# Performance work log

Hardware: AMD Instinct MI355X
Metric: run time of the kernel (lower is better)

The kernel has to match this reference:

```python
import jax, jax.numpy as jnp
import numpy as np

NUM_HEADS = 8

def setup_inputs() -> dict:
    key = jax.random.key(0)
    ks = jax.random.split(key, 7)
    B, H, W, C = 4, 56, 56, 256
    Nq = 1
    std = 0.02
    return {
        "x": jax.random.normal(ks[0], (B, H, W, C), jnp.float32),
        "cls_token": jax.random.normal(ks[1], (B, Nq, C), jnp.float32),
        "qkv_w": jax.random.normal(ks[2], (3 * C, C), jnp.float32) * std,
        "proj_w": jax.random.normal(ks[3], (C, C), jnp.float32) * std,
        "proj_b": jnp.zeros((C,), jnp.float32),
        "lepe_w": jax.random.normal(ks[4], (C, 1, 5, 5), jnp.float32) * std,
        "lepe_b": jnp.zeros((C,), jnp.float32),
    }

def reference(x, cls_token, qkv_w, proj_w, proj_b, lepe_w, lepe_b):
    B, H, W, C = x.shape
    N = H * W
    Nq = cls_token.shape[1]
    hd = C // NUM_HEADS
    scale = hd ** -0.5

    x_seq = x.reshape(B, N, C)
    x_cat = jnp.concatenate([cls_token, x_seq], axis=1)        # [B, Nq+N, C]

    qkv = x_cat @ qkv_w.T                                      # [B, Nq+N, 3C]
    qkv = qkv.reshape(B, Nq + N, 3, NUM_HEADS, hd)
    q, k, v = qkv[:, :, 0], qkv[:, :, 1], qkv[:, :, 2]         # [B, S, h, d]

    attn = jnp.einsum('bshd,bthd->bhst', q, k) * scale         # [B, h, S, S]
    attn = jax.nn.softmax(attn, axis=-1)
    out = jnp.einsum('bhst,bthd->bshd', attn, v).reshape(B, Nq + N, C)

    cls_out, x_out = out[:, :Nq], out[:, Nq:]

    # depthwise conv LePE on the raw spatial input
    x_nchw = jnp.transpose(x, (0, 3, 1, 2))                    # [B, C, H, W]
    lepe = jax.lax.conv_general_dilated(
        x_nchw, lepe_w, window_strides=(1, 1), padding='SAME',
        feature_group_count=C,
        dimension_numbers=('NCHW', 'OIHW', 'NCHW'))
    lepe = lepe + lepe_b[None, :, None, None]
    lepe = jnp.transpose(lepe, (0, 2, 3, 1)).reshape(B, N, C)

    x_out = (x_out + lepe) @ proj_w.T + proj_b
    cls_out = cls_out @ proj_w.T + proj_b
    return x_out.reshape(B, H, W, C), cls_out
```

## Files before the change

### kernel.cpp

```cpp
#include <hip/hip_runtime.h>
#include <math.h>

#define BB 4
#define HH 56
#define WW 56
#define CC 256
#define NN 3136
#define SS 3137
#define NH 8
#define HD 32
#define M_ROWS (BB * SS)
#define SPAD 3200
#define QSCALE (0.17677669529663687f * 1.4426950408889634f)
#define KT 128

typedef short short8 __attribute__((ext_vector_type(8)));
typedef short bf4    __attribute__((ext_vector_type(4)));
typedef float f32x4  __attribute__((ext_vector_type(4)));

static __device__ __forceinline__ unsigned short f2bf(float f) {
    union { float f; unsigned u; } a; a.f = f;
    unsigned r = a.u + 0x7FFF + ((a.u >> 16) & 1);
    return (unsigned short)(r >> 16);
}
static __device__ __forceinline__ float bf2f(unsigned short h) {
    union { unsigned u; float f; } a; a.u = ((unsigned)h) << 16; return a.f;
}

__global__ __launch_bounds__(256)
void pre(const float* __restrict__ cls, const float* __restrict__ qkv_w,
         const float* __restrict__ proj_w, const float* __restrict__ lepe_w,
         unsigned short* __restrict__ xb, unsigned short* __restrict__ wb,
         unsigned short* __restrict__ pwhi, unsigned short* __restrict__ pwlo,
         unsigned short* __restrict__ vt, float* __restrict__ wt,
         unsigned short* __restrict__ lepe)
{
    const int B0 = 192;
    const int B1 = B0 + 64;
    const int B2 = B1 + 64;
    const int B3 = B2 + 25;
    int blk = blockIdx.x, tid = threadIdx.x;
    if (blk < B0) {
        int row = blk * 4 + (tid >> 6);
        int c0 = (tid & 63) * 4;
        float4 v = *(const float4*)(qkv_w + (size_t)row * CC + c0);
        bf4 pk;
        pk[0] = (short)f2bf(v.x); pk[1] = (short)f2bf(v.y);
        pk[2] = (short)f2bf(v.z); pk[3] = (short)f2bf(v.w);
        *(bf4*)(wb + (size_t)row * CC + c0) = pk;
    } else if (blk < B1) {
        int row = (blk - B0) * 4 + (tid >> 6);
        int c0 = (tid & 63) * 4;
        float4 v = *(const float4*)(proj_w + (size_t)row * CC + c0);
        bf4 ph, pl;
        float vv[4] = {v.x, v.y, v.z, v.w};
        #pragma unroll
        for (int e = 0; e < 4; ++e) {
            unsigned short h = f2bf(vv[e]);
            ph[e] = (short)h;
            pl[e] = (short)f2bf(vv[e] - bf2f(h));
        }
        *(bf4*)(pwhi + (size_t)row * CC + c0) = ph;
        *(bf4*)(pwlo + (size_t)row * CC + c0) = pl;
    } else if (blk < B2) {
        int idx = blk - B1;
        int row = idx * 16 + (tid >> 4);
        int col = 3136 + (tid & 15) * 4;
        bf4 z = {};
        *(bf4*)(vt + (size_t)row * SPAD + col) = z;
    } else if (blk < B3) {
        int t = blk - B2;
        wt[(size_t)t * CC + tid] = lepe_w[(size_t)tid * 25 + t];
    } else {
        int b = blk - B3;
        xb[((size_t)b * SS) * CC + tid] = f2bf(cls[(size_t)b * CC + tid]);
        lepe[((size_t)b * SS) * CC + tid] = 0;
    }
}

__global__ __launch_bounds__(256)
void lepe_tiled(const float* __restrict__ x,
                const float* __restrict__ wt, const float* __restrict__ bias,
                unsigned short* __restrict__ lepe, unsigned short* __restrict__ xb)
{
    __shared__ unsigned short Xs[144][72];
    __shared__ float Wls[25][68];

    const int tid = threadIdx.x;
    const int bid = blockIdx.x;
    const int sp  = bid % 49;
    const int ct  = (bid / 49) & 3;
    const int b   = bid / 196;
    const int y0 = (sp / 7) * 8, x0 = (sp % 7) * 8;
    const int c0 = ct * 64;

    const int cq = tid & 15;
    const int pg = tid >> 4;

    #pragma unroll
    for (int r = 0; r < 9; ++r) {
        int seg = r * 16 + pg;
        int dy = seg / 12, dx = seg % 12;
        int yy = y0 + dy - 2, xc = x0 + dx - 2;
        bf4 v = {};
        if (yy >= 0 && yy < HH && xc >= 0 && xc < WW) {
            float4 f = *(const float4*)(x + (((size_t)b * HH + yy) * WW + xc) * CC
                                        + c0 + cq * 4);
            v[0] = (short)f2bf(f.x); v[1] = (short)f2bf(f.y);
            v[2] = (short)f2bf(f.z); v[3] = (short)f2bf(f.w);
        }
        *(bf4*)&Xs[seg][cq * 4] = v;
    }
    for (int idx = tid; idx < 1600; idx += 256) {
        int t = idx >> 6, c = idx & 63;
        Wls[t][c] = wt[(size_t)t * CC + c0 + c];
    }
    __syncthreads();

    float4 bq = *(const float4*)(bias + c0 + cq * 4);
    f32x4 acc[4];
    #pragma unroll
    for (int it = 0; it < 4; ++it) {
        acc[it][0] = bq.x; acc[it][1] = bq.y; acc[it][2] = bq.z; acc[it][3] = bq.w;
    }
    int hbase[4];
    #pragma unroll
    for (int it = 0; it < 4; ++it) {
        int pos = it * 16 + pg;
        hbase[it] = (pos >> 3) * 12 + (pos & 7);
    }

    #pragma unroll
    for (int it = 0; it < 4; ++it) {
        int pos = it * 16 + pg;
        int py = pos >> 3, px = pos & 7;
        uint2 dv = *(const uint2*)&Xs[(py + 2) * 12 + (px + 2)][cq * 4];
        *(uint2*)(xb + ((size_t)(b * SS + 1 + (y0 + py) * WW + (x0 + px))) * CC
                  + c0 + cq * 4) = dv;
    }

    #pragma unroll
    for (int t = 0; t < 25; ++t) {
        int dy = t / 5, dx = t % 5;
        float4 wq = *(const float4*)&Wls[t][cq * 4];
        #pragma unroll
        for (int it = 0; it < 4; ++it) {
            const unsigned short* xp = &Xs[hbase[it] + dy * 12 + dx][cq * 4];
            uint2 dv = *(const uint2*)xp;
            float e0 = __uint_as_float(dv.x << 16);
            float e1 = __uint_as_float(dv.x & 0xFFFF0000u);
            float e2 = __uint_as_float(dv.y << 16);
            float e3 = __uint_as_float(dv.y & 0xFFFF0000u);
            acc[it][0] += e0 * wq.x; acc[it][1] += e1 * wq.y;
            acc[it][2] += e2 * wq.z; acc[it][3] += e3 * wq.w;
        }
    }

    #pragma unroll
    for (int it = 0; it < 4; ++it) {
        int pos = it * 16 + pg;
        int py = pos >> 3, px = pos & 7;
        bf4 pk;
        pk[0] = (short)f2bf(acc[it][0]); pk[1] = (short)f2bf(acc[it][1]);
        pk[2] = (short)f2bf(acc[it][2]); pk[3] = (short)f2bf(acc[it][3]);
        *(bf4*)(lepe + ((size_t)(b * SS + 1 + (y0 + py) * WW + (x0 + px))) * CC
                + c0 + cq * 4) = pk;
    }
}

__global__ __launch_bounds__(256)
void qkv_mfma(const unsigned short* __restrict__ xb,
              const unsigned short* __restrict__ wb,
              unsigned short* __restrict__ qb, unsigned short* __restrict__ kb,
              unsigned short* __restrict__ vt)
{
    __shared__ unsigned short As[64][76];
    __shared__ unsigned short Bs[128][76];
    const int tid = threadIdx.x;
    const int w = tid >> 6, lane = tid & 63, lo = lane & 15, hi = lane >> 4;
    const int b0 = blockIdx.x / 50;
    const int s0blk = (blockIdx.x % 50) * 64;
    const int col0 = blockIdx.y * 128;
    const int wm = (w & 1) * 32, wn = (w >> 1) * 64;

    f32x4 acc[2][4] = {};

    const int arow = tid >> 3, ac8 = (tid & 7) * 8;
    const int brow = tid >> 3, bc8 = (tid & 7) * 8;

    short8 avr[2], bvr[4];
    #pragma unroll
    for (int i = 0; i < 2; ++i) {
        int row = arow + i * 32;
        short8 av = {};
        if (s0blk + row < SS)
            av = *(const short8*)(xb + (size_t)(b0 * SS + s0blk + row) * CC + ac8);
        avr[i] = av;
    }
    #pragma unroll
    for (int i = 0; i < 4; ++i)
        bvr[i] = *(const short8*)(wb + (size_t)(col0 + brow + i * 32) * CC + bc8);

    for (int k0 = 0; k0 < CC; k0 += 64) {
        __syncthreads();
        #pragma unroll
        for (int i = 0; i < 2; ++i)
            *(short8*)&As[arow + i * 32][ac8] = avr[i];
        #pragma unroll
        for (int i = 0; i < 4; ++i)
            *(short8*)&Bs[brow + i * 32][bc8] = bvr[i];
        __syncthreads();

        int kn = k0 + 64;
        if (kn < CC) {
            #pragma unroll
            for (int i = 0; i < 2; ++i) {
                int row = arow + i * 32;
                short8 av = {};
                if (s0blk + row < SS)
                    av = *(const short8*)(xb + (size_t)(b0 * SS + s0blk + row) * CC + kn + ac8);
                avr[i] = av;
            }
            #pragma unroll
            for (int i = 0; i < 4; ++i)
                bvr[i] = *(const short8*)(wb + (size_t)(col0 + brow + i * 32) * CC + kn + bc8);
        }

        #pragma unroll
        for (int kk = 0; kk < 64; kk += 32) {
            short8 af[2], bf_[4];
            #pragma unroll
            for (int m = 0; m < 2; ++m)
                af[m] = *(const short8*)&As[wm + m * 16 + lo][kk + hi * 8];
            #pragma unroll
            for (int n = 0; n < 4; ++n)
                bf_[n] = *(const short8*)&Bs[wn + n * 16 + lo][kk + hi * 8];
            #pragma unroll
            for (int m = 0; m < 2; ++m)
                #pragma unroll
                for (int n = 0; n < 4; ++n)
                    acc[m][n] = __builtin_amdgcn_mfma_f32_16x16x32_bf16(
                                    af[m], bf_[n], acc[m][n], 0, 0, 0);
        }
    }

    const int part = col0 >> 8;
    if (part < 2) {
        #pragma unroll
        for (int m = 0; m < 2; ++m) {
            #pragma unroll
            for (int rr = 0; rr < 4; ++rr) {
                int s = s0blk + wm + m * 16 + hi * 4 + rr;
                if (s >= SS) continue;
                size_t r = (size_t)(b0 * SS + s);
                #pragma unroll
                for (int n = 0; n < 4; ++n) {
                    int cc = (col0 + wn + n * 16 + lo) & 255;
                    float val = acc[m][n][rr];
                    if (part == 0) qb[r * CC + cc] = f2bf(val * QSCALE);
                    else           kb[r * CC + cc] = f2bf(val);
                }
            }
        }
    } else {
        #pragma unroll
        for (int m = 0; m < 2; ++m) {
            int s0 = s0blk + wm + m * 16 + hi * 4;
            if (s0 >= SS) continue;
            bool fast = (s0 + 3 < SS);
            #pragma unroll
            for (int n = 0; n < 4; ++n) {
                int cc = (col0 + wn + n * 16 + lo) & 255;
                int hh = cc >> 5, d = cc & 31;
                unsigned short* vrow = vt + (size_t)((b0 * NH + hh) * HD + d) * SPAD;
                if (fast) {
                    bf4 pk;
                    pk[0] = (short)f2bf(acc[m][n][0]);
                    pk[1] = (short)f2bf(acc[m][n][1]);
                    pk[2] = (short)f2bf(acc[m][n][2]);
                    pk[3] = (short)f2bf(acc[m][n][3]);
                    *(bf4*)(vrow + s0) = pk;
                } else {
                    for (int rr = 0; rr < 4 && s0 + rr < SS; ++rr)
                        vrow[s0 + rr] = f2bf(acc[m][n][rr]);
                }
            }
        }
    }
}

__global__ __launch_bounds__(256)
void attn_mfma(const unsigned short* __restrict__ qb,
               const unsigned short* __restrict__ kb,
               const unsigned short* __restrict__ vt,
               const unsigned short* __restrict__ lepe,
               unsigned short* __restrict__ ohi)
{
    __shared__ unsigned short Ks[KT][44];
    __shared__ unsigned short Vts[32][140];

    const int tid  = threadIdx.x;
    const int lane = tid & 63;
    const int w    = tid >> 6;
    const int lo   = lane & 15;
    const int hi   = lane >> 4;

    const int bid = blockIdx.x;
    const int h   = bid & 7;
    const int j   = bid >> 3;
    const int qc  = j % 25;
    const int b   = j / 25;
    const int q0w = qc * 128 + w * 32;

    short8 qa[2];
    #pragma unroll
    for (int qg = 0; qg < 2; ++qg) {
        int row = min(q0w + qg * 16 + lo, SS - 1);
        qa[qg] = *(const short8*)(qb + ((size_t)(b * SS + row)) * CC + h * HD + hi * 8);
    }

    f32x4 oacc[2][2] = {};
    f32x4 dacc[2] = {};
    bf4 ones;
    ones[0] = (short)0x3F80; ones[1] = (short)0x3F80;
    ones[2] = (short)0x3F80; ones[3] = (short)0x3F80;

    const int krow = tid >> 2, kd0 = (tid & 3) * 8;
    const int vrow = tid >> 4, vk0 = (tid & 15) * 8;
    const unsigned short* kp0 = kb + ((size_t)b * SS + krow) * CC + h * HD + kd0;
    const unsigned short* vp0 = vt + ((size_t)((b * NH + h) * HD + vrow)) * SPAD + vk0;

    short8 kv0 = *(const short8*)(kp0);
    short8 kv1 = *(const short8*)(kp0 + (size_t)64 * CC);
    short8 vv0 = *(const short8*)(vp0);
    short8 vv1 = *(const short8*)(vp0 + (size_t)16 * SPAD);

    for (int k0 = 0; k0 < SPAD; k0 += KT) {
        __syncthreads();
        *(short8*)&Ks[krow][kd0]       = kv0;
        *(short8*)&Ks[64 + krow][kd0]  = kv1;
        *(short8*)&Vts[vrow][vk0]      = vv0;
        *(short8*)&Vts[16 + vrow][vk0] = vv1;
        __syncthreads();

        int kn = k0 + KT;
        if (kn < SPAD) {
            short8 z = {};
            kv0 = (kn + krow < SS)      ? *(const short8*)(kp0 + (size_t)kn * CC)        : z;
            kv1 = (kn + 64 + krow < SS) ? *(const short8*)(kp0 + (size_t)(kn + 64) * CC) : z;
            vv0 = *(const short8*)(vp0 + kn);
            vv1 = *(const short8*)(vp0 + (size_t)16 * SPAD + kn);
        }

        #pragma unroll
        for (int g = 0; g < 8; ++g) {
            short8 kf = *(const short8*)&Ks[g * 16 + lo][hi * 8];
            bf4 vf0 = *(const bf4*)&Vts[lo][g * 16 + hi * 4];
            bf4 vf1 = *(const bf4*)&Vts[16 + lo][g * 16 + hi * 4];
            #pragma unroll
            for (int qg = 0; qg < 2; ++qg) {
                f32x4 st = __builtin_amdgcn_mfma_f32_16x16x32_bf16(
                               kf, qa[qg], (f32x4){0.f, 0.f, 0.f, 0.f}, 0, 0, 0);
                float p0 = __builtin_amdgcn_exp2f(st[0]);
                float p1 = __builtin_amdgcn_exp2f(st[1]);
                float p2 = __builtin_amdgcn_exp2f(st[2]);
                float p3 = __builtin_amdgcn_exp2f(st[3]);
                unsigned u01 = __builtin_amdgcn_perm(
                    __float_as_uint(p1), __float_as_uint(p0), 0x07060302u);
                unsigned u23 = __builtin_amdgcn_perm(
                    __float_as_uint(p3), __float_as_uint(p2), 0x07060302u);
                union { unsigned u[2]; bf4 s; } pf;
                pf.u[0] = u01; pf.u[1] = u23;
                oacc[qg][0] = __builtin_amdgcn_mfma_f32_16x16x16bf16_1k(
                                  vf0, pf.s, oacc[qg][0], 0, 0, 0);
                oacc[qg][1] = __builtin_amdgcn_mfma_f32_16x16x16bf16_1k(
                                  vf1, pf.s, oacc[qg][1], 0, 0, 0);
                dacc[qg]    = __builtin_amdgcn_mfma_f32_16x16x16bf16_1k(
                                  ones, pf.s, dacc[qg], 0, 0, 0);
            }
        }
    }

    #pragma unroll
    for (int qg = 0; qg < 2; ++qg) {
        float inv = 1.f / (dacc[qg][0] - 63.f);
        int rowq = q0w + qg * 16 + lo;
        if (rowq < SS) {
            size_t base = ((size_t)(b * SS + rowq)) * CC + h * HD;
            #pragma unroll
            for (int dt = 0; dt < 2; ++dt) {
                bf4 lep = *(const bf4*)(lepe + base + dt * 16 + hi * 4);
                bf4 pk;
                #pragma unroll
                for (int r = 0; r < 4; ++r) {
                    float val = oacc[qg][dt][r] * inv + bf2f((unsigned short)lep[r]);
                    pk[r] = (short)f2bf(val);
                }
                *(bf4*)(ohi + base + dt * 16 + hi * 4) = pk;
            }
        }
    }
}

__global__ __launch_bounds__(256)
void proj_mfma(const unsigned short* __restrict__ ohi,
               const unsigned short* __restrict__ pwhi,
               const unsigned short* __restrict__ pwlo,
               const float* __restrict__ bias, float* __restrict__ out)
{
    __shared__ unsigned short Ah[64][76];
    __shared__ unsigned short Wh[64][76];
    __shared__ unsigned short Wl[64][76];
    const int tid = threadIdx.x;
    const int w = tid >> 6, lane = tid & 63, lo = lane & 15, hi = lane >> 4;
    const int row0 = blockIdx.x * 64, col0 = blockIdx.y * 64;
    const int wm = (w & 1) * 32, wn = (w >> 1) * 32;

    f32x4 acc[2][2] = {};

    const int srow = tid >> 3, sc8 = (tid & 7) * 8;

    short8 ar[2], whr[2], wlr[2];
    #pragma unroll
    for (int i = 0; i < 2; ++i) {
        int gr = row0 + srow + i * 32;
        short8 ah = {};
        if (gr < M_ROWS) ah = *(const short8*)(ohi + (size_t)gr * CC + sc8);
        ar[i] = ah;
        int wr = col0 + srow + i * 32;
        whr[i] = *(const short8*)(pwhi + (size_t)wr * CC + sc8);
        wlr[i] = *(const short8*)(pwlo + (size_t)wr * CC + sc8);
    }

    for (int k0 = 0; k0 < CC; k0 += 64) {
        __syncthreads();
        #pragma unroll
        for (int i = 0; i < 2; ++i) {
            *(short8*)&Ah[srow + i * 32][sc8] = ar[i];
            *(short8*)&Wh[srow + i * 32][sc8] = whr[i];
            *(short8*)&Wl[srow + i * 32][sc8] = wlr[i];
        }
        __syncthreads();

        int kn = k0 + 64;
        if (kn < CC) {
            #pragma unroll
            for (int i = 0; i < 2; ++i) {
                int gr = row0 + srow + i * 32;
                short8 ah = {};
                if (gr < M_ROWS) ah = *(const short8*)(ohi + (size_t)gr * CC + kn + sc8);
                ar[i] = ah;
                int wr = col0 + srow + i * 32;
                whr[i] = *(const short8*)(pwhi + (size_t)wr * CC + kn + sc8);
                wlr[i] = *(const short8*)(pwlo + (size_t)wr * CC + kn + sc8);
            }
        }

        #pragma unroll
        for (int kk = 0; kk < 64; kk += 32) {
            short8 ah[2], wh[2], wl[2];
            #pragma unroll
            for (int m = 0; m < 2; ++m)
                ah[m] = *(const short8*)&Ah[wm + m * 16 + lo][kk + hi * 8];
            #pragma unroll
            for (int n = 0; n < 2; ++n) {
                wh[n] = *(const short8*)&Wh[wn + n * 16 + lo][kk + hi * 8];
                wl[n] = *(const short8*)&Wl[wn + n * 16 + lo][kk + hi * 8];
            }
            #pragma unroll
            for (int m = 0; m < 2; ++m)
                #pragma unroll
                for (int n = 0; n < 2; ++n) {
                    acc[m][n] = __builtin_amdgcn_mfma_f32_16x16x32_bf16(
                                    ah[m], wh[n], acc[m][n], 0, 0, 0);
                    acc[m][n] = __builtin_amdgcn_mfma_f32_16x16x32_bf16(
                                    ah[m], wl[n], acc[m][n], 0, 0, 0);
                }
        }
    }

    #pragma unroll
    for (int m = 0; m < 2; ++m) {
        #pragma unroll
        for (int rr = 0; rr < 4; ++rr) {
            int r = row0 + wm + m * 16 + hi * 4 + rr;
            if (r >= M_ROWS) continue;
            int b = r / SS, s = r % SS;
            #pragma unroll
            for (int n = 0; n < 2; ++n) {
                int col = col0 + wn + n * 16 + lo;
                float val = acc[m][n][rr] + bias[col];
                if (s == 0)
                    out[(size_t)BB * NN * CC + (size_t)b * CC + col] = val;
                else
                    out[((size_t)b * NN + (s - 1)) * CC + col] = val;
            }
        }
    }
}

extern "C" void kernel_launch(void* const* d_in, const int* in_sizes, int n_in,
                              void* d_out, int out_size, void* d_ws, size_t ws_size,
                              hipStream_t stream)
{
    const float* x      = (const float*)d_in[0];
    const float* cls    = (const float*)d_in[1];
    const float* qkv_w  = (const float*)d_in[2];
    const float* proj_w = (const float*)d_in[3];
    const float* proj_b = (const float*)d_in[4];
    const float* lepe_w = (const float*)d_in[5];
    const float* lepe_b = (const float*)d_in[6];
    float* out = (float*)d_out;

    char* ws = (char*)d_ws;
    unsigned short* qb   = (unsigned short*)(ws + 0);
    unsigned short* kb   = (unsigned short*)(ws + 6424576);
    unsigned short* vt   = (unsigned short*)(ws + 12849152);
    unsigned short* xb   = (unsigned short*)(ws + 19402752);
    unsigned short* wb   = (unsigned short*)(ws + 25827328);
    unsigned short* lepe = (unsigned short*)(ws + 26220544);
    unsigned short* ohi  = (unsigned short*)(ws + 32645120);
    unsigned short* pwhi = (unsigned short*)(ws + 39069696);
    unsigned short* pwlo = (unsigned short*)(ws + 39200768);
    float*          wt   = (float*)(ws + 39331840);

    const int PRE_BLKS = 192 + 64 + 64 + 25 + 4;
    pre       <<<PRE_BLKS, 256, 0, stream>>>(cls, qkv_w, proj_w, lepe_w,
                                             xb, wb, pwhi, pwlo, vt, wt, lepe);
    lepe_tiled<<<784, 256, 0, stream>>>(x, wt, lepe_b, lepe, xb);
    qkv_mfma  <<<dim3(200, 6), 256, 0, stream>>>(xb, wb, qb, kb, vt);
    attn_mfma <<<800, 256, 0, stream>>>(qb, kb, vt, lepe, ohi);
    proj_mfma <<<dim3(197, 4), 256, 0, stream>>>(ohi, pwhi, pwlo, proj_b, out);
}
```

Before: 194.2 us.

## Stage full-K activation tile in LDS and read weights directly from global

In both the QKV and projection GEMM kernels, the whole 64x256 activation tile is loaded into shared memory once, followed by a single barrier. The weight fragments are then read straight from global memory, relying on L2/L1 caching, instead of going through a double-buffered LDS pipeline. This removes the per-K-step barriers and the weight staging in LDS. In exchange, weight loads are no longer coalesced through LDS, their latency is exposed inside the MFMA loop, and LDS use per block grows.

```diff
diff --git a/kernel.cpp b/kernel.cpp
--- a/kernel.cpp
+++ b/kernel.cpp
@@ -174,8 +174,7 @@
               unsigned short* __restrict__ qb, unsigned short* __restrict__ kb,
               unsigned short* __restrict__ vt)
 {
-    __shared__ unsigned short As[64][76];
-    __shared__ unsigned short Bs[128][76];
+    __shared__ unsigned short As[64][264];
     const int tid = threadIdx.x;
     const int w = tid >> 6, lane = tid & 63, lo = lane & 15, hi = lane >> 4;
     const int b0 = blockIdx.x / 50;
@@ -183,65 +182,34 @@
     const int col0 = blockIdx.y * 128;
     const int wm = (w & 1) * 32, wn = (w >> 1) * 64;
 
-    f32x4 acc[2][4] = {};
-
-    const int arow = tid >> 3, ac8 = (tid & 7) * 8;
-    const int brow = tid >> 3, bc8 = (tid & 7) * 8;
-
-    short8 avr[2], bvr[4];
-    #pragma unroll
-    for (int i = 0; i < 2; ++i) {
-        int row = arow + i * 32;
+    #pragma unroll
+    for (int i = 0; i < 8; ++i) {
+        int c = tid + i * 256;
+        int row = c >> 5, c8 = (c & 31) * 8;
         short8 av = {};
         if (s0blk + row < SS)
-            av = *(const short8*)(xb + (size_t)(b0 * SS + s0blk + row) * CC + ac8);
-        avr[i] = av;
-    }
-    #pragma unroll
-    for (int i = 0; i < 4; ++i)
-        bvr[i] = *(const short8*)(wb + (size_t)(col0 + brow + i * 32) * CC + bc8);
-
-    for (int k0 = 0; k0 < CC; k0 += 64) {
-        __syncthreads();
-        #pragma unroll
-        for (int i = 0; i < 2; ++i)
-            *(short8*)&As[arow + i * 32][ac8] = avr[i];
-        #pragma unroll
-        for (int i = 0; i < 4; ++i)
-            *(short8*)&Bs[brow + i * 32][bc8] = bvr[i];
-        __syncthreads();
-
-        int kn = k0 + 64;
-        if (kn < CC) {
-            #pragma unroll
-            for (int i = 0; i < 2; ++i) {
-                int row = arow + i * 32;
-                short8 av = {};
-                if (s0blk + row < SS)
-                    av = *(const short8*)(xb + (size_t)(b0 * SS + s0blk + row) * CC + kn + ac8);
-                avr[i] = av;
-            }
-            #pragma unroll
-            for (int i = 0; i < 4; ++i)
-                bvr[i] = *(const short8*)(wb + (size_t)(col0 + brow + i * 32) * CC + kn + bc8);
-        }
-
-        #pragma unroll
-        for (int kk = 0; kk < 64; kk += 32) {
-            short8 af[2], bf_[4];
-            #pragma unroll
-            for (int m = 0; m < 2; ++m)
-                af[m] = *(const short8*)&As[wm + m * 16 + lo][kk + hi * 8];
+            av = *(const short8*)(xb + (size_t)(b0 * SS + s0blk + row) * CC + c8);
+        *(short8*)&As[row][c8] = av;
+    }
+    __syncthreads();
+
+    f32x4 acc[2][4] = {};
+    #pragma unroll
+    for (int kk = 0; kk < CC; kk += 32) {
+        short8 af[2], bf_[4];
+        #pragma unroll
+        for (int m = 0; m < 2; ++m)
+            af[m] = *(const short8*)&As[wm + m * 16 + lo][kk + hi * 8];
+        #pragma unroll
+        for (int n = 0; n < 4; ++n)
+            bf_[n] = *(const short8*)(wb + (size_t)(col0 + wn + n * 16 + lo) * CC
+                                      + kk + hi * 8);
+        #pragma unroll
+        for (int m = 0; m < 2; ++m)
             #pragma unroll
             for (int n = 0; n < 4; ++n)
-                bf_[n] = *(const short8*)&Bs[wn + n * 16 + lo][kk + hi * 8];
-            #pragma unroll
-            for (int m = 0; m < 2; ++m)
-                #pragma unroll
-                for (int n = 0; n < 4; ++n)
-                    acc[m][n] = __builtin_amdgcn_mfma_f32_16x16x32_bf16(
-                                    af[m], bf_[n], acc[m][n], 0, 0, 0);
-        }
+                acc[m][n] = __builtin_amdgcn_mfma_f32_16x16x32_bf16(
+                                af[m], bf_[n], acc[m][n], 0, 0, 0);
     }
 
     const int part = col0 >> 8;
@@ -408,75 +376,45 @@
                const unsigned short* __restrict__ pwlo,
                const float* __restrict__ bias, float* __restrict__ out)
 {
-    __shared__ unsigned short Ah[64][76];
-    __shared__ unsigned short Wh[64][76];
-    __shared__ unsigned short Wl[64][76];
+    __shared__ unsigned short Ah[64][264];
     const int tid = threadIdx.x;
     const int w = tid >> 6, lane = tid & 63, lo = lane & 15, hi = lane >> 4;
     const int row0 = blockIdx.x * 64, col0 = blockIdx.y * 64;
     const int wm = (w & 1) * 32, wn = (w >> 1) * 32;
 
+    #pragma unroll
+    for (int i = 0; i < 8; ++i) {
+        int c = tid + i * 256;
+        int row = c >> 5, c8 = (c & 31) * 8;
+        int gr = row0 + row;
+        short8 ah = {};
+        if (gr < M_ROWS) ah = *(const short8*)(ohi + (size_t)gr * CC + c8);
+        *(short8*)&Ah[row][c8] = ah;
+    }
+    __syncthreads();
+
     f32x4 acc[2][2] = {};
-
-    const int srow = tid >> 3, sc8 = (tid & 7) * 8;
-
-    short8 ar[2], whr[2], wlr[2];
-    #pragma unroll
-    for (int i = 0; i < 2; ++i) {
-        int gr = row0 + srow + i * 32;
-        short8 ah = {};
-        if (gr < M_ROWS) ah = *(const short8*)(ohi + (size_t)gr * CC + sc8);
-        ar[i] = ah;
-        int wr = col0 + srow + i * 32;
-        whr[i] = *(const short8*)(pwhi + (size_t)wr * CC + sc8);
-        wlr[i] = *(const short8*)(pwlo + (size_t)wr * CC + sc8);
-    }
-
-    for (int k0 = 0; k0 < CC; k0 += 64) {
-        __syncthreads();
-        #pragma unroll
-        for (int i = 0; i < 2; ++i) {
-            *(short8*)&Ah[srow + i * 32][sc8] = ar[i];
-            *(short8*)&Wh[srow + i * 32][sc8] = whr[i];
-            *(short8*)&Wl[srow + i * 32][sc8] = wlr[i];
-        }
-        __syncthreads();
-
-        int kn = k0 + 64;
-        if (kn < CC) {
-            #pragma unroll
-            for (int i = 0; i < 2; ++i) {
-                int gr = row0 + srow + i * 32;
-                short8 ah = {};
-                if (gr < M_ROWS) ah = *(const short8*)(ohi + (size_t)gr * CC + kn + sc8);
-                ar[i] = ah;
-                int wr = col0 + srow + i * 32;
-                whr[i] = *(const short8*)(pwhi + (size_t)wr * CC + kn + sc8);
-                wlr[i] = *(const short8*)(pwlo + (size_t)wr * CC + kn + sc8);
-            }
-        }
-
-        #pragma unroll
-        for (int kk = 0; kk < 64; kk += 32) {
-            short8 ah[2], wh[2], wl[2];
-            #pragma unroll
-            for (int m = 0; m < 2; ++m)
-                ah[m] = *(const short8*)&Ah[wm + m * 16 + lo][kk + hi * 8];
+    #pragma unroll
+    for (int kk = 0; kk < CC; kk += 32) {
+        short8 ah[2], wh[2], wl[2];
+        #pragma unroll
+        for (int m = 0; m < 2; ++m)
+            ah[m] = *(const short8*)&Ah[wm + m * 16 + lo][kk + hi * 8];
+        #pragma unroll
+        for (int n = 0; n < 2; ++n) {
+            size_t wrow = (size_t)(col0 + wn + n * 16 + lo) * CC + kk + hi * 8;
+            wh[n] = *(const short8*)(pwhi + wrow);
+            wl[n] = *(const short8*)(pwlo + wrow);
+        }
+        #pragma unroll
+        for (int m = 0; m < 2; ++m)
             #pragma unroll
             for (int n = 0; n < 2; ++n) {
-                wh[n] = *(const short8*)&Wh[wn + n * 16 + lo][kk + hi * 8];
-                wl[n] = *(const short8*)&Wl[wn + n * 16 + lo][kk + hi * 8];
-            }
-            #pragma unroll
-            for (int m = 0; m < 2; ++m)
-                #pragma unroll
-                for (int n = 0; n < 2; ++n) {
-                    acc[m][n] = __builtin_amdgcn_mfma_f32_16x16x32_bf16(
-                                    ah[m], wh[n], acc[m][n], 0, 0, 0);
-                    acc[m][n] = __builtin_amdgcn_mfma_f32_16x16x32_bf16(
-                                    ah[m], wl[n], acc[m][n], 0, 0, 0);
-                }
-        }
+                acc[m][n] = __builtin_amdgcn_mfma_f32_16x16x32_bf16(
+                                ah[m], wh[n], acc[m][n], 0, 0, 0);
+                acc[m][n] = __builtin_amdgcn_mfma_f32_16x16x32_bf16(
+                                ah[m], wl[n], acc[m][n], 0, 0, 0);
+            }
     }
 
     #pragma unroll
```

After: 217.1 us. +11.8%, slower.
